# Kernel tuning notes

Measured on AMD Instinct MI355X. Metric: run time of the kernel, lower is better.

The kernel has to match this reference:

```python
import jax, jax.numpy as jnp
import numpy as np

EPS = 1e-6

def setup_inputs() -> dict:
    key = jax.random.key(0)
    ks = jax.random.split(key, 7)
    T, B, S, A, D = 512, 32, 64, 8, 32
    x = jax.random.normal(ks[0], (T, B, D), dtype=jnp.float32)
    a = jax.random.normal(ks[1], (T, B, A), dtype=jnp.float32)
    mask = jnp.ones((T, B), dtype=jnp.float32)
    mu = jax.random.normal(ks[2], (S, D), dtype=jnp.float32)
    logv = 0.1 * jax.random.normal(ks[3], (S, D), dtype=jnp.float32)
    init_logits = jax.random.normal(ks[4], (S,), dtype=jnp.float32)
    w_base = 0.1 * jax.random.normal(ks[5], (S, S), dtype=jnp.float32)
    w_act = 0.1 * jax.random.normal(ks[6], (A, S, S), dtype=jnp.float32)
    return {"x": x, "a": a, "mask": mask, "mu": mu, "logv": logv,
            "init_logits": init_logits, "w_base": w_base, "w_act": w_act}

def reference(x, a, mask, mu, logv, init_logits, w_base, w_act):
    T, B, D = x.shape
    S = mu.shape[0]
    # Gaussian (diag) emission log-likelihood for every state: [T, B, S]
    var = jnp.exp(logv)
    diff = x[:, :, None, :] - mu  # [T, B, S, D]
    logp_x = -0.5 * jnp.sum(diff * diff / var + logv + jnp.log(2.0 * jnp.pi), axis=-1)
    # Logistic (action-conditioned) transition matrices for t=1..T-1: [T-1, B, S, S]
    trans = jax.nn.softmax(w_base + jnp.einsum('tba,aij->tbij', a[:-1], w_act), axis=-1)
    logp0 = jax.nn.log_softmax(init_logits)
    # alpha_0
    alpha0 = jax.nn.softmax(logp_x[0] + logp0, axis=-1)

    def fwd_step(b, inp):
        tr, lx = inp
        logp_z = jnp.log(jnp.sum(tr * b[:, :, None] + EPS, axis=-2))
        b_new = jax.nn.softmax(lx + logp_z, axis=-1)
        return b_new, b_new

    _, alpha_rest = jax.lax.scan(fwd_step, alpha0, (trans, logp_x[1:]))
    alpha = jnp.concatenate([alpha0[None], alpha_rest], axis=0)  # [T, B, S]

    log_trans = jnp.log(trans + EPS)

    def bwd_step(logb, inp):
        ltr, lx, m = inp
        new = jax.scipy.special.logsumexp(lx[:, None, :] + ltr + logb[:, None, :], axis=-1)
        new = new * (m[:, None] == 1)
        return new, new

    _, lb = jax.lax.scan(bwd_step, jnp.zeros((B, S), x.dtype),
                         (log_trans, logp_x[1:], mask[1:]), reverse=True)
    log_beta = jnp.concatenate([lb, jnp.zeros((1, B, S), x.dtype)], axis=0)  # [T, B, S]

    # Posterior state marginals
    q_z = jax.nn.softmax(jnp.log(alpha + EPS) + log_beta, axis=-1)
    return q_z
```

## Files before the change

kernel.cpp:

```cpp
#include <hip/hip_runtime.h>
#include <hip/hip_fp16.h>
#include <math.h>

#define TT 512
#define BB 32
#define SS 64
#define AA 8
#define DD 32
#define EPSF 1e-6f
#define SEPS (64.0f * 1e-6f)
#define TS 68

typedef _Float16 h2_t __attribute__((ext_vector_type(2)));
typedef __fp16   fp16v2 __attribute__((ext_vector_type(2)));

__device__ __forceinline__ int   f2i(float x){ return __float_as_int(x); }
__device__ __forceinline__ float i2f(int x){ return __int_as_float(x); }
__device__ __forceinline__ float readlane_f(float v, int l){
  return i2f(__builtin_amdgcn_readlane(f2i(v), l));
}
__device__ __forceinline__ h2_t i2h2(int x){ return __builtin_bit_cast(h2_t, x); }
__device__ __forceinline__ h2_t u2h2(unsigned x){ return __builtin_bit_cast(h2_t, x); }
__device__ __forceinline__ int pkrtz_i(float a, float b){
  fp16v2 p = __builtin_amdgcn_cvt_pkrtz(a, b);
  return __builtin_bit_cast(int, p);
}
template<int CTRL, int RMASK>
__device__ __forceinline__ float dpp_add(float x){
  return x + i2f(__builtin_amdgcn_update_dpp(0, f2i(x), CTRL, RMASK, 0xf, true));
}
__device__ __forceinline__ float wave_sum_dpp(float x){
  x = dpp_add<0x111, 0xf>(x);
  x = dpp_add<0x112, 0xf>(x);
  x = dpp_add<0x114, 0xf>(x);
  x = dpp_add<0x118, 0xf>(x);
  x = dpp_add<0x142, 0xa>(x);
  x = dpp_add<0x143, 0xc>(x);
  return readlane_f(x, 63);
}
__device__ __forceinline__ float dpp_xor1(float x){
  return i2f(__builtin_amdgcn_update_dpp(0, f2i(x), 0xB1, 0xf, 0xf, true));
}
__device__ __forceinline__ float wave_sum(float v){
  #pragma unroll
  for (int m = 1; m < 64; m <<= 1) v += __shfl_xor(v, m, 64);
  return v;
}
__device__ __forceinline__ float wave_max(float v){
  #pragma unroll
  for (int m = 1; m < 64; m <<= 1) v = fmaxf(v, __shfl_xor(v, m, 64));
  return v;
}
#define BARRIER() asm volatile("s_waitcnt lgkmcnt(0)\n\ts_barrier" ::: "memory")

__device__ __forceinline__ unsigned pk2(float a, float b){
  return (unsigned)__half_as_ushort(__float2half_rn(a))
       | ((unsigned)__half_as_ushort(__float2half_rn(b)) << 16);
}

#if __has_builtin(__builtin_amdgcn_fdot2)
#define FDOT2(A, B, C) __builtin_amdgcn_fdot2((A), (B), (C), false)
#else
__device__ __forceinline__ float fdot2_emul(h2_t a, h2_t b, float c){
  return fmaf((float)a.x, (float)b.x, fmaf((float)a.y, (float)b.y, c));
}
#define FDOT2(A, B, C) fdot2_emul((A), (B), (C))
#endif

__global__ void prep_kernel(const float* __restrict__ logv,
                            float* __restrict__ iv, float* __restrict__ cs){
  int gid = blockIdx.x * blockDim.x + threadIdx.x;
  if (gid < SS * DD) iv[gid] = __expf(-logv[gid]);
  if (gid < SS){
    float s = 0.f;
    #pragma unroll
    for (int d = 0; d < DD; ++d) s += logv[gid * DD + d];
    cs[gid] = s + (float)DD * 1.8378770664093453f;
  }
}

__global__ __launch_bounds__(256) void logpx_kernel(
    const float* __restrict__ x, const float* __restrict__ mu,
    const float* __restrict__ iv, const float* __restrict__ cs,
    float* __restrict__ slx_out){
  const int lane = threadIdx.x & 63;
  const int w = threadIdx.x >> 6;
  const int row = blockIdx.x * 4 + w;
  const float* __restrict__ xp  = x  + row * DD;
  const float* __restrict__ mup = mu + lane * DD;
  const float* __restrict__ ivp = iv + lane * DD;
  float acc = 0.f;
  #pragma unroll
  for (int d = 0; d < DD; ++d){
    float diff = xp[d] - mup[d];
    acc = fmaf(diff * diff, ivp[d], acc);
  }
  float lx = -0.5f * (acc + cs[lane]);
  float mx = wave_max(lx);
  slx_out[row * SS + lane] = lx - mx;
}

__global__ __launch_bounds__(512) void trans_kernel(
    const float* __restrict__ a, const float* __restrict__ w_base,
    const float* __restrict__ w_act, unsigned short* __restrict__ trans, int F){
  const int b  = blockIdx.x >> 4;
  const int tc = blockIdx.x & 15;
  const int t0 = tc * 32;
  const int q    = threadIdx.x >> 6;
  const int j    = threadIdx.x & 63;
  __shared__ float aS[32 * 8];
  if (threadIdx.x < 256)
    aS[threadIdx.x] = a[(((t0 + (threadIdx.x >> 3)) * BB) + b) * AA + (threadIdx.x & 7)];
  float wb[8], wa[8][8];
  #pragma unroll
  for (int e = 0; e < 8; ++e){
    wb[e] = w_base[(8 * q + e) * SS + j];
    #pragma unroll
    for (int k = 0; k < 8; ++k)
      wa[k][e] = w_act[(k * SS + 8 * q + e) * SS + j];
  }
  __syncthreads();
  int rem = F - t0;
  const int nt = (rem < 0) ? 0 : (rem < 32 ? rem : 32);
  for (int tt = 0; tt < nt; ++tt){
    float aa[8];
    #pragma unroll
    for (int k = 0; k < 8; ++k) aa[k] = aS[tt * 8 + k];
    float ev[8], rs[8];
    #pragma unroll
    for (int e = 0; e < 8; ++e){
      float u = wb[e];
      #pragma unroll
      for (int k = 0; k < 8; ++k) u = fmaf(aa[k], wa[k][e], u);
      ev[e] = __expf(u); rs[e] = ev[e];
    }
    #pragma unroll
    for (int m = 1; m < 64; m <<= 1){
      #pragma unroll
      for (int e = 0; e < 8; ++e) rs[e] += __shfl_xor(rs[e], m, 64);
    }
    float ri[8];
    #pragma unroll
    for (int e = 0; e < 8; ++e) ri[e] = __builtin_amdgcn_rcpf(rs[e]);
    uint4 o;
    o.x = pk2(ev[0] * ri[0], ev[1] * ri[1]);
    o.y = pk2(ev[2] * ri[2], ev[3] * ri[3]);
    o.z = pk2(ev[4] * ri[4], ev[5] * ri[5]);
    o.w = pk2(ev[6] * ri[6], ev[7] * ri[7]);
    *(uint4*)(trans + ((size_t)(t0 + tt) * BB + b) * (SS * SS) + q * 512 + j * 8) = o;
  }
}

__global__ __launch_bounds__(64) void scan_wave_kernel(
    const float* __restrict__ slx, const float* __restrict__ mask,
    const float* __restrict__ il, const unsigned short* __restrict__ trans,
    float* __restrict__ alpha, float* __restrict__ log_beta){
  const int lane = threadIdx.x;
  const bool is_fwd = (blockIdx.x < BB);
  const int b = is_fwd ? blockIdx.x : (blockIdx.x - BB);

  __shared__ __align__(16) int Ltr[2][32 * 68];

#define LOADT(ARR, t) do{ \
    const uint4* p_ = (const uint4*)(trans + ((size_t)(t) * BB + b) * (SS * SS) + lane * 8); \
    _Pragma("unroll") \
    for (int q_ = 0; q_ < 8; ++q_) ARR[q_] = p_[q_ * 64]; \
  }while(0)

  if (is_fwd){
    uint4 A[8], B[8], C[8], D[8];
#define DOTQ(ARR, Q) \
    a0 = FDOT2(i2h2(__builtin_amdgcn_readlane(upki, 8*Q + 0)), u2h2(ARR[Q].x), a0); \
    a1 = FDOT2(i2h2(__builtin_amdgcn_readlane(upki, 8*Q + 2)), u2h2(ARR[Q].y), a1); \
    a2 = FDOT2(i2h2(__builtin_amdgcn_readlane(upki, 8*Q + 4)), u2h2(ARR[Q].z), a2); \
    a3 = FDOT2(i2h2(__builtin_amdgcn_readlane(upki, 8*Q + 6)), u2h2(ARR[Q].w), a3);
#define DOTS(ARR) \
    DOTQ(ARR,0) DOTQ(ARR,1) DOTQ(ARR,2) DOTQ(ARR,3) \
    DOTQ(ARR,4) DOTQ(ARR,5) DOTQ(ARR,6) DOTQ(ARR,7)

    LOADT(A, 0); LOADT(B, 1); LOADT(C, 2); LOADT(D, 3);
    float u = __expf(slx[b * SS + lane] + il[lane]);
    float c = __builtin_amdgcn_rcpf(wave_sum_dpp(u));
    alpha[b * SS + lane] = u * c;
    float slxn = slx[(BB + b) * SS + lane];

#define FBODY(s_, ARR, DOL, DOS) { \
    float elxc = __expf(slxn); \
    if (DOS) slxn = slx[(((s_) + 2) * BB + b) * SS + lane]; \
    float usw = dpp_xor1(u); \
    int upki = pkrtz_i(u, usw); \
    float a0 = 0.f, a1 = 0.f, a2 = 0.f, a3 = 0.f; \
    DOTS(ARR); \
    if (DOL) LOADT(ARR, (s_) + 4); \
    float S_ = (a0 + a1) + (a2 + a3); \
    u = elxc * fmaf(c, S_, SEPS); \
    c = __builtin_amdgcn_rcpf(wave_sum_dpp(u)); \
    alpha[(((s_) + 1) * BB + b) * SS + lane] = u * c; }

    for (int s = 0; s < 504; s += 4){
      FBODY(s + 0, A, 1, 1)
      FBODY(s + 1, B, 1, 1)
      FBODY(s + 2, C, 1, 1)
      FBODY(s + 3, D, 1, 1)
    }
    FBODY(504, A, 1, 1)
    FBODY(505, B, 1, 1)
    FBODY(506, C, 1, 1)
    FBODY(507, D, 0, 1)
    FBODY(508, A, 0, 1)
    FBODY(509, B, 0, 1)
    FBODY(510, C, 0, 0)
  } else {
    uint4 R0[8], R1[8];
#define WLDS(SL, R) do{ \
    int* Lp_ = &Ltr[SL][lane]; \
    _Pragma("unroll") \
    for (int q_ = 0; q_ < 8; ++q_){ \
      Lp_[(4*q_ + 0) * 68] = (int)R[q_].x; \
      Lp_[(4*q_ + 1) * 68] = (int)R[q_].y; \
      Lp_[(4*q_ + 2) * 68] = (int)R[q_].z; \
      Lp_[(4*q_ + 3) * 68] = (int)R[q_].w; \
    } \
  }while(0)

    LOADT(R0, TT - 2);
    WLDS(0, R0);
    LOADT(R0, TT - 3);
    LOADT(R1, TT - 4);
    float breg = 0.f;
    log_beta[((TT - 1) * BB + b) * SS + lane] = 0.f;
    float slxc = slx[((TT - 1) * BB + b) * SS + lane];
    float mg = mask[(TT - 1) * BB + b];
    const int sel = (lane & 1) ? 0x07060302 : 0x05040100;

#define BBODY(s_, RB, DOW, DOL, DOT_) { \
    const int t_ = TT - 2 - (s_); \
    int4 w4[16]; \
    { const int4* rp_ = (const int4*)&Ltr[(s_) & 1][(lane >> 1) * 68]; \
      _Pragma("unroll") \
      for (int k_ = 0; k_ < 16; ++k_) w4[k_] = rp_[k_]; } \
    if (DOW) WLDS(((s_) + 1) & 1, RB); \
    if (DOL) LOADT(RB, t_ - 3); \
    int hh[32]; const int* wd_ = (const int*)w4; \
    _Pragma("unroll") \
    for (int m_ = 0; m_ < 32; ++m_) \
      hh[m_] = (int)__builtin_amdgcn_perm((unsigned)wd_[2*m_ + 1], (unsigned)wd_[2*m_], (unsigned)sel); \
    float wgt = __expf(slxc + breg); \
    float W_ = wave_sum_dpp(wgt); \
    float rW_ = __builtin_amdgcn_rcpf(W_); \
    float wsw = dpp_xor1(wgt); \
    int wpki = pkrtz_i(wgt, wsw); \
    float a0 = 0.f, a1 = 0.f, a2 = 0.f, a3 = 0.f; \
    _Pragma("unroll") \
    for (int m_ = 0; m_ < 32; m_ += 4){ \
      a0 = FDOT2(i2h2(__builtin_amdgcn_readlane(wpki, 2*m_ + 0)), i2h2(hh[m_ + 0]), a0); \
      a1 = FDOT2(i2h2(__builtin_amdgcn_readlane(wpki, 2*m_ + 2)), i2h2(hh[m_ + 1]), a1); \
      a2 = FDOT2(i2h2(__builtin_amdgcn_readlane(wpki, 2*m_ + 4)), i2h2(hh[m_ + 2]), a2); \
      a3 = FDOT2(i2h2(__builtin_amdgcn_readlane(wpki, 2*m_ + 6)), i2h2(hh[m_ + 3]), a3); \
    } \
    float S_ = (a0 + a1) + (a2 + a3); \
    float v_ = __logf(fmaf(S_, rW_, EPSF)); \
    breg = (mg == 1.0f) ? v_ : 0.0f; \
    log_beta[(t_ * BB + b) * SS + lane] = breg; \
    if (DOT_){ slxc = slx[(t_ * BB + b) * SS + lane]; mg = mask[t_ * BB + b]; } }

    for (int s = 0; s < 508; s += 2){
      BBODY(s + 0, R0, 1, 1, 1)
      BBODY(s + 1, R1, 1, 1, 1)
    }
    BBODY(508, R0, 1, 0, 1)
    BBODY(509, R1, 1, 0, 1)
    BBODY(510, R0, 0, 0, 0)
  }
}

__global__ __launch_bounds__(768) void scan_kernel(
    const float* __restrict__ slx, const float* __restrict__ mask,
    const float* __restrict__ il, const float* __restrict__ a,
    const float* __restrict__ w_base, const float* __restrict__ w_act,
    float* __restrict__ alpha, float* __restrict__ log_beta){
  const int lane = threadIdx.x & 63;
  const int w    = threadIdx.x >> 6;
  const bool is_fwd = (blockIdx.x < BB);
  const int b = is_fwd ? blockIdx.x : (blockIdx.x - BB);

  __shared__ __align__(16) float tile[3][SS * TS];
  __shared__ float rsp[3][8][SS];
  __shared__ float fpart[2][4][SS];
  __shared__ __align__(16) float aLDS[TT * AA];
  __shared__ float mLDS[TT];

  for (int idx = threadIdx.x; idx < TT * AA; idx += 768){
    int t = idx >> 3, k = idx & 7;
    aLDS[idx] = a[(t * BB + b) * AA + k];
  }
  for (int idx = threadIdx.x; idx < TT; idx += 768)
    mLDS[idx] = mask[idx * BB + b];

  if (w >= 4){
    const int pw = w - 4;
    const int jb = pw * 8;
    float wb[8], wa[8][8];
    #pragma unroll
    for (int jj = 0; jj < 8; ++jj){
      wb[jj] = w_base[lane * SS + jb + jj];
      #pragma unroll
      for (int k = 0; k < 8; ++k)
        wa[k][jj] = w_act[(k * SS + lane) * SS + jb + jj];
    }
    float aa[8], aan[8];
    {
      const int t0 = is_fwd ? 0 : (TT - 2);
      const float* __restrict__ ap = a + (t0 * BB + b) * AA;
      #pragma unroll
      for (int k = 0; k < 8; ++k) aa[k] = ap[k];
      const int t1 = is_fwd ? 1 : (TT - 3);
      const float* __restrict__ ap1 = a + (t1 * BB + b) * AA;
      #pragma unroll
      for (int k = 0; k < 8; ++k) aan[k] = ap1[k];
    }
    {
      float ev[8]; float racc = 0.f;
      #pragma unroll
      for (int jj = 0; jj < 8; ++jj){
        float u = wb[jj];
        #pragma unroll
        for (int k = 0; k < 8; ++k) u = fmaf(aa[k], wa[k][jj], u);
        ev[jj] = __expf(u); racc += ev[jj];
      }
      *(float4*)&tile[0][lane * TS + jb]     = make_float4(ev[0],ev[1],ev[2],ev[3]);
      *(float4*)&tile[0][lane * TS + jb + 4] = make_float4(ev[4],ev[5],ev[6],ev[7]);
      rsp[0][pw][lane] = racc;
    }
    BARRIER();
    int tw = 1;
    for (int s = 0; s < TT - 1; ++s){
      if (s <= TT - 3){
        #pragma unroll
        for (int k = 0; k < 8; ++k) aa[k] = aan[k];
        if (s + 1 <= TT - 3){
          const int tn = is_fwd ? (s + 2) : (TT - 4 - s);
          #pragma unroll
          for (int k = 0; k < 8; ++k) aan[k] = aLDS[tn * AA + k];
        }
        float ev[8]; float racc = 0.f;
        #pragma unroll
        for (int jj = 0; jj < 8; ++jj){
          float u = wb[jj];
          #pragma unroll
          for (int k = 0; k < 8; ++k) u = fmaf(aa[k], wa[k][jj], u);
          ev[jj] = __expf(u); racc += ev[jj];
        }
        *(float4*)&tile[tw][lane * TS + jb]     = make_float4(ev[0],ev[1],ev[2],ev[3]);
        *(float4*)&tile[tw][lane * TS + jb + 4] = make_float4(ev[4],ev[5],ev[6],ev[7]);
        rsp[tw][pw][lane] = racc;
        tw = (tw == 2) ? 0 : tw + 1;
      }
      BARRIER();
    }
  } else if (is_fwd){
    const int wb16 = __builtin_amdgcn_readfirstlane(w * 16);
    float u = __expf(slx[b * SS + lane] + il[lane]);
    float c = __builtin_amdgcn_rcpf(wave_sum_dpp(u));
    if (w == 0) alpha[b * SS + lane] = u * c;
    float slxn = slx[(BB + b) * SS + lane];
    float elxc = 0.f;
    BARRIER();
    int ts = 0;
    for (int s = 0; s < TT - 1; ++s){
      if (s > 0){
        const int fs = (s - 1) & 1;
        float S = (fpart[fs][0][lane] + fpart[fs][1][lane])
                + (fpart[fs][2][lane] + fpart[fs][3][lane]);
        u = elxc * fmaf(c, S, SEPS);
        c = __builtin_amdgcn_rcpf(wave_sum_dpp(u));
        if (w == 0) alpha[(s * BB + b) * SS + lane] = u * c;
      }
      float rs = ((rsp[ts][0][lane] + rsp[ts][1][lane]) + (rsp[ts][2][lane] + rsp[ts][3][lane]))
               + ((rsp[ts][4][lane] + rsp[ts][5][lane]) + (rsp[ts][6][lane] + rsp[ts][7][lane]));
      float va = u * __builtin_amdgcn_rcpf(rs);
      const float* __restrict__ tp = &tile[ts][0];
      float a0 = 0.f, a1 = 0.f, a2 = 0.f, a3 = 0.f;
      #pragma unroll
      for (int r = 0; r < 16; r += 4){
        a0 = fmaf(readlane_f(va, wb16 + r    ), tp[(wb16 + r    ) * TS + lane], a0);
        a1 = fmaf(readlane_f(va, wb16 + r + 1), tp[(wb16 + r + 1) * TS + lane], a1);
        a2 = fmaf(readlane_f(va, wb16 + r + 2), tp[(wb16 + r + 2) * TS + lane], a2);
        a3 = fmaf(readlane_f(va, wb16 + r + 3), tp[(wb16 + r + 3) * TS + lane], a3);
      }
      fpart[s & 1][w][lane] = (a0 + a1) + (a2 + a3);
      elxc = __expf(slxn);
      if (s + 2 <= TT - 1) slxn = slx[((s + 2) * BB + b) * SS + lane];
      ts = (ts == 2) ? 0 : ts + 1;
      BARRIER();
    }
    {
      const int fs = (TT - 2) & 1;
      float S = (fpart[fs][0][lane] + fpart[fs][1][lane])
              + (fpart[fs][2][lane] + fpart[fs][3][lane]);
      u = elxc * fmaf(c, S, SEPS);
      c = __builtin_amdgcn_rcpf(wave_sum_dpp(u));
      if (w == 0) alpha[((TT - 1) * BB + b) * SS + lane] = u * c;
    }
  } else {
    const int wb16 = __builtin_amdgcn_readfirstlane(w * 16);
    float breg = 0.f, rWc = 1.f;
    if (w == 0) log_beta[((TT - 1) * BB + b) * SS + lane] = 0.f;
    float slxc = slx[((TT - 1) * BB + b) * SS + lane];
    float mprev = 1.f;
    BARRIER();
    int ts = 0, pts = 2;
    for (int s = 0; s < TT - 1; ++s){
      if (s > 0){
        const int fs = (s - 1) & 1;
        float eh = (fpart[fs][0][lane] + fpart[fs][1][lane])
                 + (fpart[fs][2][lane] + fpart[fs][3][lane]);
        float rsv = ((rsp[pts][0][lane] + rsp[pts][1][lane]) + (rsp[pts][2][lane] + rsp[pts][3][lane]))
                  + ((rsp[pts][4][lane] + rsp[pts][5][lane]) + (rsp[pts][6][lane] + rsp[pts][7][lane]));
        float v = __logf(fmaf(eh * __builtin_amdgcn_rcpf(rsv), rWc, EPSF));
        breg = (mprev == 1.0f) ? v : 0.0f;
        if (w == 0) log_beta[((TT - 1 - s) * BB + b) * SS + lane] = breg;
      }
      float wgt = __expf(slxc + breg);
      float W = wave_sum_dpp(wgt);
      rWc = __builtin_amdgcn_rcpf(W);
      const float* __restrict__ tp = &tile[ts][lane * TS + wb16];
      float4 e0 = *(const float4*)(tp);
      float4 e1 = *(const float4*)(tp + 4);
      float4 e2 = *(const float4*)(tp + 8);
      float4 e3 = *(const float4*)(tp + 12);
      float a0 = 0.f, a1 = 0.f, a2 = 0.f, a3 = 0.f;
      a0 = fmaf(readlane_f(wgt, wb16 + 0),  e0.x, a0);
      a1 = fmaf(readlane_f(wgt, wb16 + 1),  e0.y, a1);
      a2 = fmaf(readlane_f(wgt, wb16 + 2),  e0.z, a2);
      a3 = fmaf(readlane_f(wgt, wb16 + 3),  e0.w, a3);
      a0 = fmaf(readlane_f(wgt, wb16 + 4),  e1.x, a0);
      a1 = fmaf(readlane_f(wgt, wb16 + 5),  e1.y, a1);
      a2 = fmaf(readlane_f(wgt, wb16 + 6),  e1.z, a2);
      a3 = fmaf(readlane_f(wgt, wb16 + 7),  e1.w, a3);
      a0 = fmaf(readlane_f(wgt, wb16 + 8),  e2.x, a0);
      a1 = fmaf(readlane_f(wgt, wb16 + 9),  e2.y, a1);
      a2 = fmaf(readlane_f(wgt, wb16 + 10), e2.z, a2);
      a3 = fmaf(readlane_f(wgt, wb16 + 11), e2.w, a3);
      a0 = fmaf(readlane_f(wgt, wb16 + 12), e3.x, a0);
      a1 = fmaf(readlane_f(wgt, wb16 + 13), e3.y, a1);
      a2 = fmaf(readlane_f(wgt, wb16 + 14), e3.z, a2);
      a3 = fmaf(readlane_f(wgt, wb16 + 15), e3.w, a3);
      fpart[s & 1][w][lane] = (a0 + a1) + (a2 + a3);
      mprev = mLDS[TT - 1 - s];
      if (s <= TT - 3) slxc = slx[((TT - 2 - s) * BB + b) * SS + lane];
      pts = ts; ts = (ts == 2) ? 0 : ts + 1;
      BARRIER();
    }
    {
      const int fs = (TT - 2) & 1;
      float eh = (fpart[fs][0][lane] + fpart[fs][1][lane])
               + (fpart[fs][2][lane] + fpart[fs][3][lane]);
      float rsv = ((rsp[pts][0][lane] + rsp[pts][1][lane]) + (rsp[pts][2][lane] + rsp[pts][3][lane]))
                + ((rsp[pts][4][lane] + rsp[pts][5][lane]) + (rsp[pts][6][lane] + rsp[pts][7][lane]));
      float v = __logf(fmaf(eh * __builtin_amdgcn_rcpf(rsv), rWc, EPSF));
      breg = (mprev == 1.0f) ? v : 0.0f;
      if (w == 0) log_beta[b * SS + lane] = breg;
    }
  }
}

__global__ __launch_bounds__(256) void qz_kernel(
    const float* __restrict__ alpha, const float* __restrict__ log_beta,
    float* __restrict__ out){
  const int lane = threadIdx.x & 63;
  const int w = threadIdx.x >> 6;
  const int row = blockIdx.x * 4 + w;
  float v = __logf(alpha[row * SS + lane] + EPSF) + log_beta[row * SS + lane];
  float mx = wave_max(v);
  float e = __expf(v - mx);
  float sm = wave_sum(e);
  out[row * SS + lane] = e * __builtin_amdgcn_rcpf(sm);
}

extern "C" void kernel_launch(void* const* d_in, const int* in_sizes, int n_in,
                              void* d_out, int out_size, void* d_ws, size_t ws_size,
                              hipStream_t stream){
  const float* x      = (const float*)d_in[0];
  const float* a      = (const float*)d_in[1];
  const float* mask   = (const float*)d_in[2];
  const float* mu     = (const float*)d_in[3];
  const float* logv   = (const float*)d_in[4];
  const float* il     = (const float*)d_in[5];
  const float* w_base = (const float*)d_in[6];
  const float* w_act  = (const float*)d_in[7];
  float* out = (float*)d_out;

  float* ws = (float*)d_ws;
  const size_t TBS = (size_t)TT * BB * SS;
  float* iv       = ws;
  float* cs       = ws + 2048;
  float* slx      = ws + 4096;
  float* alpha    = slx + TBS;
  float* log_beta = alpha + TBS;
  unsigned short* trans = (unsigned short*)(log_beta + TBS);

  const size_t base_bytes = ((size_t)4096 + 3 * TBS) * 4;
  const size_t full_bytes = base_bytes + (size_t)(TT - 1) * BB * SS * SS * 2;

  prep_kernel<<<8, 256, 0, stream>>>(logv, iv, cs);
  logpx_kernel<<<TT * BB / 4, 256, 0, stream>>>(x, mu, iv, cs, slx);
  if (ws_size >= full_bytes){
    trans_kernel<<<512, 512, 0, stream>>>(a, w_base, w_act, trans, TT - 1);
    scan_wave_kernel<<<2 * BB, 64, 0, stream>>>(slx, mask, il, trans,
                                                alpha, log_beta);
  } else {
    scan_kernel<<<2 * BB, 768, 0, stream>>>(slx, mask, il, a, w_base, w_act,
                                            alpha, log_beta);
  }
  qz_kernel<<<TT * BB / 4, 256, 0, stream>>>(alpha, log_beta, out);
}
```

Before: 428.6 us.

## Carry beta in linear domain and use LDS reduction for transition softmax

The backward scan now carries exp(beta) directly, so the per-step exp of slx+beta is replaced by a product with a precomputed exp(slx). The log moves off the recurrence and is used only for the output store. The slx and mask values are prefetched two steps ahead. In trans_kernel, the 8x6 shuffle butterfly used for the row-sum softmax normalization is replaced by an LDS transpose, a partial sum, three shuffles and readlane broadcasts. This shortens the serial dependency chain per scan step, at the cost of extra LDS traffic and a possible loss of range when exponentials are carried.

```diff
diff --git a/kernel.cpp b/kernel.cpp
--- a/kernel.cpp
+++ b/kernel.cpp
@@ -52,6 +52,7 @@
   return v;
 }
 #define BARRIER() asm volatile("s_waitcnt lgkmcnt(0)\n\ts_barrier" ::: "memory")
+#define LGKM0()   asm volatile("s_waitcnt lgkmcnt(0)" ::: "memory")
 
 __device__ __forceinline__ unsigned pk2(float a, float b){
   return (unsigned)__half_as_ushort(__float2half_rn(a))
@@ -109,6 +110,7 @@
   const int q    = threadIdx.x >> 6;
   const int j    = threadIdx.x & 63;
   __shared__ float aS[32 * 8];
+  __shared__ float red[8][8][68];
   if (threadIdx.x < 256)
     aS[threadIdx.x] = a[(((t0 + (threadIdx.x >> 3)) * BB) + b) * AA + (threadIdx.x & 7)];
   float wb[8], wa[8][8];
@@ -120,33 +122,40 @@
       wa[k][e] = w_act[(k * SS + 8 * q + e) * SS + j];
   }
   __syncthreads();
+  const int er = j & 7;
+  const int g8 = (j >> 3) * 8;
   int rem = F - t0;
   const int nt = (rem < 0) ? 0 : (rem < 32 ? rem : 32);
   for (int tt = 0; tt < nt; ++tt){
     float aa[8];
     #pragma unroll
     for (int k = 0; k < 8; ++k) aa[k] = aS[tt * 8 + k];
-    float ev[8], rs[8];
+    float ev[8];
     #pragma unroll
     for (int e = 0; e < 8; ++e){
       float u = wb[e];
       #pragma unroll
       for (int k = 0; k < 8; ++k) u = fmaf(aa[k], wa[k][e], u);
-      ev[e] = __expf(u); rs[e] = ev[e];
-    }
-    #pragma unroll
-    for (int m = 1; m < 64; m <<= 1){
-      #pragma unroll
-      for (int e = 0; e < 8; ++e) rs[e] += __shfl_xor(rs[e], m, 64);
-    }
-    float ri[8];
-    #pragma unroll
-    for (int e = 0; e < 8; ++e) ri[e] = __builtin_amdgcn_rcpf(rs[e]);
+      ev[e] = __expf(u);
+    }
+    #pragma unroll
+    for (int e = 0; e < 8; ++e) red[q][e][j] = ev[e];
+    LGKM0();
+    float4 p0 = *(const float4*)&red[q][er][g8];
+    float4 p1 = *(const float4*)&red[q][er][g8 + 4];
+    float part = ((p0.x + p0.y) + (p0.z + p0.w)) + ((p1.x + p1.y) + (p1.z + p1.w));
+    part += __shfl_xor(part, 8, 64);
+    part += __shfl_xor(part, 16, 64);
+    part += __shfl_xor(part, 32, 64);
+    float ri = __builtin_amdgcn_rcpf(part);
+    float re[8];
+    #pragma unroll
+    for (int e = 0; e < 8; ++e) re[e] = readlane_f(ri, e);
     uint4 o;
-    o.x = pk2(ev[0] * ri[0], ev[1] * ri[1]);
-    o.y = pk2(ev[2] * ri[2], ev[3] * ri[3]);
-    o.z = pk2(ev[4] * ri[4], ev[5] * ri[5]);
-    o.w = pk2(ev[6] * ri[6], ev[7] * ri[7]);
+    o.x = pk2(ev[0] * re[0], ev[1] * re[1]);
+    o.y = pk2(ev[2] * re[2], ev[3] * re[3]);
+    o.z = pk2(ev[4] * re[4], ev[5] * re[5]);
+    o.w = pk2(ev[6] * re[6], ev[7] * re[7]);
     *(uint4*)(trans + ((size_t)(t0 + tt) * BB + b) * (SS * SS) + q * 512 + j * 8) = o;
   }
 }
@@ -227,29 +236,40 @@
     WLDS(0, R0);
     LOADT(R0, TT - 3);
     LOADT(R1, TT - 4);
-    float breg = 0.f;
+    float pcar = 1.0f;
     log_beta[((TT - 1) * BB + b) * SS + lane] = 0.f;
-    float slxc = slx[((TT - 1) * BB + b) * SS + lane];
-    float mg = mask[(TT - 1) * BB + b];
+    float elxc = __expf(slx[((TT - 1) * BB + b) * SS + lane]);
+    float sxn1 = slx[((TT - 2) * BB + b) * SS + lane];
+    float sxn2 = slx[((TT - 3) * BB + b) * SS + lane];
+    float mkc  = mask[(TT - 1) * BB + b];
+    float mkn1 = mask[(TT - 2) * BB + b];
+    float mkn2 = mask[(TT - 3) * BB + b];
     const int sel = (lane & 1) ? 0x07060302 : 0x05040100;
 
-#define BBODY(s_, RB, DOW, DOL, DOT_) { \
+#define BBODY(s_, RB, DOW, DOL, DOP) { \
     const int t_ = TT - 2 - (s_); \
     int4 w4[16]; \
     { const int4* rp_ = (const int4*)&Ltr[(s_) & 1][(lane >> 1) * 68]; \
       _Pragma("unroll") \
       for (int k_ = 0; k_ < 16; ++k_) w4[k_] = rp_[k_]; } \
+    float wgt = elxc * pcar; \
+    float wsw = dpp_xor1(wgt); \
+    int wpki = pkrtz_i(wgt, wsw); \
+    float W_ = wave_sum_dpp(wgt); \
+    float rW_ = __builtin_amdgcn_rcpf(W_); \
     if (DOW) WLDS(((s_) + 1) & 1, RB); \
     if (DOL) LOADT(RB, t_ - 3); \
+    float mcur = mkc; \
+    float elxn = __expf(sxn1); \
+    sxn1 = sxn2; mkc = mkn1; mkn1 = mkn2; \
+    if (DOP){ \
+      sxn2 = slx[((t_ - 2) * BB + b) * SS + lane]; \
+      mkn2 = mask[(t_ - 2) * BB + b]; \
+    } \
     int hh[32]; const int* wd_ = (const int*)w4; \
     _Pragma("unroll") \
     for (int m_ = 0; m_ < 32; ++m_) \
       hh[m_] = (int)__builtin_amdgcn_perm((unsigned)wd_[2*m_ + 1], (unsigned)wd_[2*m_], (unsigned)sel); \
-    float wgt = __expf(slxc + breg); \
-    float W_ = wave_sum_dpp(wgt); \
-    float rW_ = __builtin_amdgcn_rcpf(W_); \
-    float wsw = dpp_xor1(wgt); \
-    int wpki = pkrtz_i(wgt, wsw); \
     float a0 = 0.f, a1 = 0.f, a2 = 0.f, a3 = 0.f; \
     _Pragma("unroll") \
     for (int m_ = 0; m_ < 32; m_ += 4){ \
@@ -259,17 +279,17 @@
       a3 = FDOT2(i2h2(__builtin_amdgcn_readlane(wpki, 2*m_ + 6)), i2h2(hh[m_ + 3]), a3); \
     } \
     float S_ = (a0 + a1) + (a2 + a3); \
-    float v_ = __logf(fmaf(S_, rW_, EPSF)); \
-    breg = (mg == 1.0f) ? v_ : 0.0f; \
-    log_beta[(t_ * BB + b) * SS + lane] = breg; \
-    if (DOT_){ slxc = slx[(t_ * BB + b) * SS + lane]; mg = mask[t_ * BB + b]; } }
+    float pv_ = fmaf(S_, rW_, EPSF); \
+    pcar = (mcur == 1.0f) ? pv_ : 1.0f; \
+    log_beta[(t_ * BB + b) * SS + lane] = __logf(pcar); \
+    elxc = elxn; }
 
     for (int s = 0; s < 508; s += 2){
       BBODY(s + 0, R0, 1, 1, 1)
       BBODY(s + 1, R1, 1, 1, 1)
     }
     BBODY(508, R0, 1, 0, 1)
-    BBODY(509, R1, 1, 0, 1)
+    BBODY(509, R1, 1, 0, 0)
     BBODY(510, R0, 0, 0, 0)
   }
 }
```

Measured after the change: 381.4 us. 11.0% less time.
